# Performance work log

Hardware: AMD Instinct MI355X
Metric: run time of the kernel (lower is better)

Reference implementation:

```python
import jax, jax.numpy as jnp
import numpy as np
from jax.scipy.linalg import solve_triangular

B, N = 8192, 1024  # patch batch, neighborhood size; order=3 -> 10 jet coefficients


def setup_inputs() -> dict:
    key = jax.random.key(0)
    k1, k2 = jax.random.split(key)
    points = jax.random.normal(k1, (B, 3, N), dtype=jnp.float32)
    weights = jax.random.uniform(k2, (B, N), dtype=jnp.float32)
    return {"points": points, "weights": weights}


def fit_wjet_order3(points, weights):
    # points: [B,3,N], weights: [B,N]
    bsz, _, n = points.shape
    x = points[:, 0, :, None]  # [B,N,1]
    y = points[:, 1, :, None]
    z = points[:, 2, :, None]
    w = weights[:, :, None]                      # [B,N,1]
    valid_count = jnp.sum(w > 0.001, axis=1)     # [B,1]
    w_vec = jnp.where(valid_count > 18, weights, jnp.ones_like(weights))[:, :, None]  # [B,N,1]

    # scale normalization h (order > 1 branch)
    h = (jnp.mean(jnp.abs(x), axis=1) + jnp.mean(jnp.abs(y), axis=1)) / 2.0  # [B,1]
    h = jnp.where(jnp.abs(h) < 0.0001, 0.1, h)
    hh = h[:, :, None]                            # [B,1,1]
    x = x / hh
    y = y / hh

    # order-3 polynomial feature matrix A: [B,N,10]
    x_2 = x * x
    y_2 = y * y
    xy = x * y
    A = jnp.concatenate([x, y, x_2, y_2, xy, x_2 * x, y_2 * y, x_2 * y, y_2 * x,
                         jnp.ones_like(x)], axis=2)
    h_2 = h * h
    h_3 = h_2 * h
    d_inv = 1.0 / jnp.concatenate([h, h, h_2, h_2, h_2, h_3, h_3, h_3, h_3,
                                   jnp.ones_like(h)], axis=1)  # [B,10]

    # normal equations (weighted): XtX [B,10,10], XtY [B,10,1]
    XtX = jnp.einsum('bnm,bnk->bmk', A, w_vec * A)
    XtY = jnp.einsum('bnm,bnk->bmk', A, w_vec * z)

    # batched Cholesky solve (happy path of solve_linear_system)
    L = jnp.linalg.cholesky(XtX)
    u = solve_triangular(L, XtY, lower=True)
    beta = solve_triangular(jnp.swapaxes(L, -1, -2), u, lower=False)  # [B,10,1]

    beta = d_inv[:, :, None] * beta  # D_inv @ beta (D_inv is diagonal)

    ones_b1 = jnp.ones((bsz, 1), dtype=beta.dtype)
    n_est = jnp.concatenate([-beta[:, 0:2, 0], ones_b1], axis=1)
    n_est = n_est / jnp.linalg.norm(n_est, axis=1, keepdims=True)

    # analytic neighbor normals (order == 3)
    def bk(k):
        return beta[:, k][:, None, :]  # [B,1,1] broadcasts over N
    nx = -(bk(0) + 2 * bk(2) * x + bk(4) * y + 3 * bk(5) * x_2 + 2 * bk(7) * xy + bk(8) * y_2)
    ny = -(bk(1) + 2 * bk(3) * y + bk(4) * x + 3 * bk(6) * y_2 + bk(7) * x_2 + 2 * bk(8) * xy)
    nn_ = jnp.concatenate([nx, ny, jnp.ones((bsz, n, 1), dtype=beta.dtype)], axis=2)  # [B,N,3]
    neighbor_normals = nn_ / jnp.linalg.norm(nn_, axis=2, keepdims=True)

    return beta[:, :, 0], n_est, neighbor_normals


def reference(points, weights):
    return fit_wjet_order3(points, weights)
```

## Files before the change

kernel.cpp:

```cpp
#include <hip/hip_runtime.h>
#include <math.h>

#define NPTS 1024
#define THREADS 256

template <int CTRL>
__device__ __forceinline__ float dpp_add(float v) {
  int m = __builtin_amdgcn_update_dpp(0, __builtin_bit_cast(int, v), CTRL, 0xF, 0xF, true);
  return v + __builtin_bit_cast(float, m);
}

__device__ __forceinline__ float row_red16(float v) {
  v = dpp_add<0x111>(v);
  v = dpp_add<0x112>(v);
  v = dpp_add<0x114>(v);
  v = dpp_add<0x118>(v);
  return v;
}

__device__ __forceinline__ double rl_f64(double v, int l) {
  typedef int v2i __attribute__((ext_vector_type(2)));
  v2i u = __builtin_bit_cast(v2i, v);
  v2i r;
  r.x = __builtin_amdgcn_readlane(u.x, l);
  r.y = __builtin_amdgcn_readlane(u.y, l);
  return __builtin_bit_cast(double, r);
}

__device__ __forceinline__ float bperm_f(int srclane, float v) {
  return __builtin_bit_cast(float,
      __builtin_amdgcn_ds_bpermute(srclane << 2, __builtin_bit_cast(int, v)));
}

__global__ void __launch_bounds__(THREADS) deepfit_kernel(
    const float* __restrict__ pts, const float* __restrict__ wts,
    float* __restrict__ beta_out, float* __restrict__ nest_out,
    float* __restrict__ nn_out)
{
  const int b = blockIdx.x;
  const int t = threadIdx.x;
  const int lane = t & 63;
  const int wid = t >> 6;

  __shared__ __attribute__((aligned(16))) float s_red[39][16];
  __shared__ int s_cnt[4];
  __shared__ int s_redo;
  __shared__ float s_hw;
  __shared__ float s_beta[10];
  __shared__ double s_L[100];

  const float4* px4 = reinterpret_cast<const float4*>(pts + (size_t)b * (3 * NPTS));
  const float4* pw4 = reinterpret_cast<const float4*>(wts + (size_t)b * NPTS);

  float4 x4 = px4[t];
  float4 y4 = px4[THREADS + t];
  float4 z4 = px4[2 * THREADS + t];
  float4 w4 = pw4[t];

  float xv[4] = {x4.x, x4.y, x4.z, x4.w};
  float yv[4] = {y4.x, y4.y, y4.z, y4.w};
  float zv[4] = {z4.x, z4.y, z4.z, z4.w};
  float wv[4] = {w4.x, w4.y, w4.z, w4.w};

  float habs = 0.f;
  int cnt = 0;
#pragma unroll
  for (int p = 0; p < 4; ++p) {
    habs += fabsf(xv[p]) + fabsf(yv[p]);
    cnt += (int)__popcll(__ballot(wv[p] > 0.001f));
  }
  habs = row_red16(habs);
  if ((lane & 15) == 15) s_red[38][wid * 4 + (lane >> 4)] = habs;
  if (lane == 0) s_cnt[wid] = cnt;

  bool wone = false;
  for (int it = 0; it < 2; ++it) {
    float M[28], Z[10];
#pragma unroll
    for (int i = 0; i < 28; ++i) M[i] = 0.f;
#pragma unroll
    for (int i = 0; i < 10; ++i) Z[i] = 0.f;

#pragma unroll
    for (int p = 0; p < 4; ++p) {
      float x = xv[p];
      float y = yv[p];
      float w = wone ? 1.0f : wv[p];
      float wz = w * zv[p];
      float yp1 = y, yp2 = y * y, yp3 = yp2 * y, yp4 = yp3 * y, yp5 = yp4 * y, yp6 = yp5 * y;
      float tx = w;
      M[0] += tx; M[1] += tx * yp1; M[2] += tx * yp2; M[3] += tx * yp3; M[4] += tx * yp4; M[5] += tx * yp5; M[6] += tx * yp6;
      tx *= x;
      M[7] += tx; M[8] += tx * yp1; M[9] += tx * yp2; M[10] += tx * yp3; M[11] += tx * yp4; M[12] += tx * yp5;
      tx *= x;
      M[13] += tx; M[14] += tx * yp1; M[15] += tx * yp2; M[16] += tx * yp3; M[17] += tx * yp4;
      tx *= x;
      M[18] += tx; M[19] += tx * yp1; M[20] += tx * yp2; M[21] += tx * yp3;
      tx *= x;
      M[22] += tx; M[23] += tx * yp1; M[24] += tx * yp2;
      tx *= x;
      M[25] += tx; M[26] += tx * yp1;
      tx *= x;
      M[27] += tx;
      float tz = wz;
      Z[0] += tz; Z[1] += tz * yp1; Z[2] += tz * yp2; Z[3] += tz * yp3;
      tz *= x;
      Z[4] += tz; Z[5] += tz * yp1; Z[6] += tz * yp2;
      tz *= x;
      Z[7] += tz; Z[8] += tz * yp1;
      tz *= x;
      Z[9] += tz;
    }

#pragma unroll
    for (int i = 0; i < 28; ++i) {
      float v = row_red16(M[i]);
      if ((lane & 15) == 15) s_red[i][wid * 4 + (lane >> 4)] = v;
    }
#pragma unroll
    for (int i = 0; i < 10; ++i) {
      float v = row_red16(Z[i]);
      if ((lane & 15) == 15) s_red[28 + i][wid * 4 + (lane >> 4)] = v;
    }
    __syncthreads();

    if (wid == 0) {
      float rowsum = 0.f;
      if (lane < 39) {
        const float4* r4 = reinterpret_cast<const float4*>(&s_red[lane][0]);
        float4 a0 = r4[0], a1 = r4[1], a2 = r4[2], a3 = r4[3];
        rowsum = ((a0.x + a0.y) + (a0.z + a0.w)) + ((a1.x + a1.y) + (a1.z + a1.w)) +
                 ((a2.x + a2.y) + (a2.z + a2.w)) + ((a3.x + a3.y) + (a3.z + a3.w));
      }
      int ctot = s_cnt[0] + s_cnt[1] + s_cnt[2] + s_cnt[3];
      float hs = __builtin_bit_cast(float,
          __builtin_amdgcn_readlane(__builtin_bit_cast(int, rowsum), 38));
      float mh = hs * (1.0f / 2048.0f);
      if (fabsf(mh) < 1e-4f) mh = 0.1f;
      bool redo = (it == 0) && (ctot <= 18);
      if (lane == 0) { s_redo = redo ? 1 : 0; s_hw = mh; }

      if (!redo) {
        const int lc = (lane < 10) ? lane : 0;
        const int axi = (0x18D21u >> (2 * lc)) & 3;
        const int ayi = (0x27184u >> (2 * lc)) & 3;
        constexpr int AXC[10] = {1, 0, 2, 0, 1, 3, 0, 2, 1, 0};
        constexpr int AYC[10] = {0, 1, 0, 2, 1, 0, 3, 1, 2, 0};
        double a[10], yy;
#pragma unroll
        for (int j = 0; j < 10; ++j) {
          int as = axi + AXC[j];
          int bs = ayi + AYC[j];
          int idx = as * 7 - (as * (as - 1)) / 2 + bs;
          a[j] = (double)bperm_f(idx, rowsum);
        }
        {
          int zi = axi * 4 - (axi * (axi - 1)) / 2 + ayi;
          yy = (double)bperm_f(28 + zi, rowsum);
        }

        if (lane < 10) {
          double Lc[10];
          double rd_own = 1.0;
#pragma unroll
          for (int j = 0; j < 10; ++j) {
            double dj = rl_f64(a[j], j);
            double rdj = 1.0 / dj;
            double lij = a[j] * rdj;
            Lc[j] = lij;
            if (lane == j) rd_own = rdj;
            double wj = rl_f64(yy, j);
            if (lane > j) yy -= lij * wj;
#pragma unroll
            for (int k = j + 1; k < 10; ++k) {
              double ajk = rl_f64(a[k], j);
              a[k] -= lij * ajk;
            }
          }
          yy *= rd_own;
#pragma unroll
          for (int j = 0; j < 10; ++j) s_L[lane * 10 + j] = Lc[j];
          asm volatile("s_waitcnt lgkmcnt(0)" ::: "memory");
#pragma unroll
          for (int j = 9; j >= 0; --j) {
            double xj = rl_f64(yy, j);
            if (lane < j) yy -= s_L[j * 10 + lane] * xj;
          }
          float bf = (float)yy;
          s_beta[lane] = bf;
          beta_out[(size_t)b * 10 + lane] = bf;
          double b0 = rl_f64(yy, 0);
          double b1 = rl_f64(yy, 1);
          if (lane == 0) {
            double invn = 1.0 / sqrt(b0 * b0 + b1 * b1 + 1.0);
            nest_out[(size_t)b * 3 + 0] = (float)(-b0 * invn);
            nest_out[(size_t)b * 3 + 1] = (float)(-b1 * invn);
            nest_out[(size_t)b * 3 + 2] = (float)invn;
          }
        }
      }
    }
    __syncthreads();
    if (s_redo == 0) break;
    wone = true;
  }

  const float h = s_hw;
  const float inv_h = 1.0f / h;
  float bb[10];
#pragma unroll
  for (int i = 0; i < 10; ++i) bb[i] = s_beta[i];
  float nx[4], ny[4], nz[4];
#pragma unroll
  for (int p = 0; p < 4; ++p) {
    float x = xv[p] * inv_h;
    float y = yv[p] * inv_h;
    float x2 = x * x, y2 = y * y, xy = x * y;
    float vx = -(bb[0] + 2.f * bb[2] * x + bb[4] * y + 3.f * bb[5] * x2 + 2.f * bb[7] * xy + bb[8] * y2);
    float vy = -(bb[1] + 2.f * bb[3] * y + bb[4] * x + 3.f * bb[6] * y2 + bb[7] * x2 + 2.f * bb[8] * xy);
    float invn = 1.0f / sqrtf(vx * vx + vy * vy + 1.0f);
    nx[p] = vx * invn; ny[p] = vy * invn; nz[p] = invn;
  }
  {
    float4* o4 = reinterpret_cast<float4*>(nn_out + (size_t)b * (NPTS * 3));
    float4 f0 = make_float4(nx[0], ny[0], nz[0], nx[1]);
    float4 f1 = make_float4(ny[1], nz[1], nx[2], ny[2]);
    float4 f2 = make_float4(nz[2], nx[3], ny[3], nz[3]);
    o4[3 * t + 0] = f0;
    o4[3 * t + 1] = f1;
    o4[3 * t + 2] = f2;
  }
}

extern "C" void kernel_launch(void* const* d_in, const int* in_sizes, int n_in,
                              void* d_out, int out_size, void* d_ws, size_t ws_size,
                              hipStream_t stream) {
  const float* pts = (const float*)d_in[0];
  const float* wts = (const float*)d_in[1];
  float* out = (float*)d_out;
  const int B = in_sizes[1] / NPTS;
  float* beta_out = out;
  float* nest_out = out + (size_t)B * 10;
  float* nn_out = out + (size_t)B * 13;
  deepfit_kernel<<<B, THREADS, 0, stream>>>(pts, wts, beta_out, nest_out, nn_out);
}
```

Measured before the change: 56.08 us.

## Map one patch per wavefront and drop block-level syncs and shared reductions

Each wavefront now handles a whole patch, with four patches per block, instead of a 256-thread block per patch. Reductions use full-wave DPP plus readlane instead of shared-memory partials and __syncthreads. The redo pass re-reads inputs from global memory, and the normal-evaluation stage reloads x and y rather than keeping them in registers. This removes block barriers and the serialized single-wave solve, but makes each lane do four times more accumulation work and adds repeated global loads.

```diff
diff --git a/kernel.cpp b/kernel.cpp
--- a/kernel.cpp
+++ b/kernel.cpp
@@ -2,7 +2,8 @@
 #include <math.h>
 
 #define NPTS 1024
-#define THREADS 256
+#define WPB 4
+#define THREADS (64 * WPB)
 
 template <int CTRL>
 __device__ __forceinline__ float dpp_add(float v) {
@@ -10,12 +11,19 @@
   return v + __builtin_bit_cast(float, m);
 }
 
-__device__ __forceinline__ float row_red16(float v) {
+__device__ __forceinline__ float wave_red_full(float v) {
   v = dpp_add<0x111>(v);
   v = dpp_add<0x112>(v);
   v = dpp_add<0x114>(v);
   v = dpp_add<0x118>(v);
+  v = dpp_add<0x142>(v);
+  v = dpp_add<0x143>(v);
   return v;
+}
+
+__device__ __forceinline__ float red_total(float v) {
+  return __builtin_bit_cast(float,
+      __builtin_amdgcn_readlane(__builtin_bit_cast(int, wave_red_full(v)), 63));
 }
 
 __device__ __forceinline__ double rl_f64(double v, int l) {
@@ -35,200 +43,187 @@
 __global__ void __launch_bounds__(THREADS) deepfit_kernel(
     const float* __restrict__ pts, const float* __restrict__ wts,
     float* __restrict__ beta_out, float* __restrict__ nest_out,
-    float* __restrict__ nn_out)
+    float* __restrict__ nn_out, int B)
 {
-  const int b = blockIdx.x;
-  const int t = threadIdx.x;
-  const int lane = t & 63;
-  const int wid = t >> 6;
-
-  __shared__ __attribute__((aligned(16))) float s_red[39][16];
-  __shared__ int s_cnt[4];
-  __shared__ int s_redo;
-  __shared__ float s_hw;
-  __shared__ float s_beta[10];
-  __shared__ double s_L[100];
+  const int lane = threadIdx.x & 63;
+  const int wid = threadIdx.x >> 6;
+  const int b = blockIdx.x * WPB + wid;
+  if (b >= B) return;
+
+  __shared__ double s_L[WPB][100];
+  double* sL = &s_L[wid][0];
 
   const float4* px4 = reinterpret_cast<const float4*>(pts + (size_t)b * (3 * NPTS));
   const float4* pw4 = reinterpret_cast<const float4*>(wts + (size_t)b * NPTS);
 
-  float4 x4 = px4[t];
-  float4 y4 = px4[THREADS + t];
-  float4 z4 = px4[2 * THREADS + t];
-  float4 w4 = pw4[t];
-
-  float xv[4] = {x4.x, x4.y, x4.z, x4.w};
-  float yv[4] = {y4.x, y4.y, y4.z, y4.w};
-  float zv[4] = {z4.x, z4.y, z4.z, z4.w};
-  float wv[4] = {w4.x, w4.y, w4.z, w4.w};
-
+  float M[28], Z[10];
   float habs = 0.f;
   int cnt = 0;
-#pragma unroll
-  for (int p = 0; p < 4; ++p) {
-    habs += fabsf(xv[p]) + fabsf(yv[p]);
-    cnt += (int)__popcll(__ballot(wv[p] > 0.001f));
-  }
-  habs = row_red16(habs);
-  if ((lane & 15) == 15) s_red[38][wid * 4 + (lane >> 4)] = habs;
-  if (lane == 0) s_cnt[wid] = cnt;
-
-  bool wone = false;
-  for (int it = 0; it < 2; ++it) {
-    float M[28], Z[10];
+
+  for (int pass = 0; pass < 2; ++pass) {
 #pragma unroll
     for (int i = 0; i < 28; ++i) M[i] = 0.f;
 #pragma unroll
     for (int i = 0; i < 10; ++i) Z[i] = 0.f;
 
 #pragma unroll
-    for (int p = 0; p < 4; ++p) {
-      float x = xv[p];
-      float y = yv[p];
-      float w = wone ? 1.0f : wv[p];
-      float wz = w * zv[p];
-      float yp1 = y, yp2 = y * y, yp3 = yp2 * y, yp4 = yp3 * y, yp5 = yp4 * y, yp6 = yp5 * y;
-      float tx = w;
-      M[0] += tx; M[1] += tx * yp1; M[2] += tx * yp2; M[3] += tx * yp3; M[4] += tx * yp4; M[5] += tx * yp5; M[6] += tx * yp6;
-      tx *= x;
-      M[7] += tx; M[8] += tx * yp1; M[9] += tx * yp2; M[10] += tx * yp3; M[11] += tx * yp4; M[12] += tx * yp5;
-      tx *= x;
-      M[13] += tx; M[14] += tx * yp1; M[15] += tx * yp2; M[16] += tx * yp3; M[17] += tx * yp4;
-      tx *= x;
-      M[18] += tx; M[19] += tx * yp1; M[20] += tx * yp2; M[21] += tx * yp3;
-      tx *= x;
-      M[22] += tx; M[23] += tx * yp1; M[24] += tx * yp2;
-      tx *= x;
-      M[25] += tx; M[26] += tx * yp1;
-      tx *= x;
-      M[27] += tx;
-      float tz = wz;
-      Z[0] += tz; Z[1] += tz * yp1; Z[2] += tz * yp2; Z[3] += tz * yp3;
-      tz *= x;
-      Z[4] += tz; Z[5] += tz * yp1; Z[6] += tz * yp2;
-      tz *= x;
-      Z[7] += tz; Z[8] += tz * yp1;
-      tz *= x;
-      Z[9] += tz;
-    }
-
-#pragma unroll
-    for (int i = 0; i < 28; ++i) {
-      float v = row_red16(M[i]);
-      if ((lane & 15) == 15) s_red[i][wid * 4 + (lane >> 4)] = v;
-    }
-#pragma unroll
-    for (int i = 0; i < 10; ++i) {
-      float v = row_red16(Z[i]);
-      if ((lane & 15) == 15) s_red[28 + i][wid * 4 + (lane >> 4)] = v;
-    }
-    __syncthreads();
-
-    if (wid == 0) {
-      float rowsum = 0.f;
-      if (lane < 39) {
-        const float4* r4 = reinterpret_cast<const float4*>(&s_red[lane][0]);
-        float4 a0 = r4[0], a1 = r4[1], a2 = r4[2], a3 = r4[3];
-        rowsum = ((a0.x + a0.y) + (a0.z + a0.w)) + ((a1.x + a1.y) + (a1.z + a1.w)) +
-                 ((a2.x + a2.y) + (a2.z + a2.w)) + ((a3.x + a3.y) + (a3.z + a3.w));
-      }
-      int ctot = s_cnt[0] + s_cnt[1] + s_cnt[2] + s_cnt[3];
-      float hs = __builtin_bit_cast(float,
-          __builtin_amdgcn_readlane(__builtin_bit_cast(int, rowsum), 38));
-      float mh = hs * (1.0f / 2048.0f);
-      if (fabsf(mh) < 1e-4f) mh = 0.1f;
-      bool redo = (it == 0) && (ctot <= 18);
-      if (lane == 0) { s_redo = redo ? 1 : 0; s_hw = mh; }
-
-      if (!redo) {
-        const int lc = (lane < 10) ? lane : 0;
-        const int axi = (0x18D21u >> (2 * lc)) & 3;
-        const int ayi = (0x27184u >> (2 * lc)) & 3;
-        constexpr int AXC[10] = {1, 0, 2, 0, 1, 3, 0, 2, 1, 0};
-        constexpr int AYC[10] = {0, 1, 0, 2, 1, 0, 3, 1, 2, 0};
-        double a[10], yy;
-#pragma unroll
-        for (int j = 0; j < 10; ++j) {
-          int as = axi + AXC[j];
-          int bs = ayi + AYC[j];
-          int idx = as * 7 - (as * (as - 1)) / 2 + bs;
-          a[j] = (double)bperm_f(idx, rowsum);
-        }
-        {
-          int zi = axi * 4 - (axi * (axi - 1)) / 2 + ayi;
-          yy = (double)bperm_f(28 + zi, rowsum);
-        }
-
-        if (lane < 10) {
-          double Lc[10];
-          double rd_own = 1.0;
-#pragma unroll
-          for (int j = 0; j < 10; ++j) {
-            double dj = rl_f64(a[j], j);
-            double rdj = 1.0 / dj;
-            double lij = a[j] * rdj;
-            Lc[j] = lij;
-            if (lane == j) rd_own = rdj;
-            double wj = rl_f64(yy, j);
-            if (lane > j) yy -= lij * wj;
-#pragma unroll
-            for (int k = j + 1; k < 10; ++k) {
-              double ajk = rl_f64(a[k], j);
-              a[k] -= lij * ajk;
-            }
-          }
-          yy *= rd_own;
-#pragma unroll
-          for (int j = 0; j < 10; ++j) s_L[lane * 10 + j] = Lc[j];
-          asm volatile("s_waitcnt lgkmcnt(0)" ::: "memory");
-#pragma unroll
-          for (int j = 9; j >= 0; --j) {
-            double xj = rl_f64(yy, j);
-            if (lane < j) yy -= s_L[j * 10 + lane] * xj;
-          }
-          float bf = (float)yy;
-          s_beta[lane] = bf;
-          beta_out[(size_t)b * 10 + lane] = bf;
-          double b0 = rl_f64(yy, 0);
-          double b1 = rl_f64(yy, 1);
-          if (lane == 0) {
-            double invn = 1.0 / sqrt(b0 * b0 + b1 * b1 + 1.0);
-            nest_out[(size_t)b * 3 + 0] = (float)(-b0 * invn);
-            nest_out[(size_t)b * 3 + 1] = (float)(-b1 * invn);
-            nest_out[(size_t)b * 3 + 2] = (float)invn;
-          }
+    for (int c = 0; c < 4; ++c) {
+      float4 x4 = px4[lane + 64 * c];
+      float4 y4 = px4[256 + lane + 64 * c];
+      float4 z4 = px4[512 + lane + 64 * c];
+      float4 w4 = pw4[lane + 64 * c];
+      float xs[4] = {x4.x, x4.y, x4.z, x4.w};
+      float ys[4] = {y4.x, y4.y, y4.z, y4.w};
+      float zs[4] = {z4.x, z4.y, z4.z, z4.w};
+      float ws[4] = {w4.x, w4.y, w4.z, w4.w};
+      if (pass == 0) {
+#pragma unroll
+        for (int p = 0; p < 4; ++p) {
+          habs += fabsf(xs[p]) + fabsf(ys[p]);
+          cnt += (int)__popcll(__ballot(ws[p] > 0.001f));
         }
       }
-    }
-    __syncthreads();
-    if (s_redo == 0) break;
-    wone = true;
-  }
-
-  const float h = s_hw;
-  const float inv_h = 1.0f / h;
+#pragma unroll
+      for (int p = 0; p < 4; ++p) {
+        float x = xs[p], y = ys[p];
+        float w = (pass == 0) ? ws[p] : 1.0f;
+        float wz = w * zs[p];
+        float yp1 = y, yp2 = y * y, yp3 = yp2 * y, yp4 = yp3 * y, yp5 = yp4 * y, yp6 = yp5 * y;
+        float tx = w;
+        M[0] += tx; M[1] += tx * yp1; M[2] += tx * yp2; M[3] += tx * yp3; M[4] += tx * yp4; M[5] += tx * yp5; M[6] += tx * yp6;
+        tx *= x;
+        M[7] += tx; M[8] += tx * yp1; M[9] += tx * yp2; M[10] += tx * yp3; M[11] += tx * yp4; M[12] += tx * yp5;
+        tx *= x;
+        M[13] += tx; M[14] += tx * yp1; M[15] += tx * yp2; M[16] += tx * yp3; M[17] += tx * yp4;
+        tx *= x;
+        M[18] += tx; M[19] += tx * yp1; M[20] += tx * yp2; M[21] += tx * yp3;
+        tx *= x;
+        M[22] += tx; M[23] += tx * yp1; M[24] += tx * yp2;
+        tx *= x;
+        M[25] += tx; M[26] += tx * yp1;
+        tx *= x;
+        M[27] += tx;
+        float tz = wz;
+        Z[0] += tz; Z[1] += tz * yp1; Z[2] += tz * yp2; Z[3] += tz * yp3;
+        tz *= x;
+        Z[4] += tz; Z[5] += tz * yp1; Z[6] += tz * yp2;
+        tz *= x;
+        Z[7] += tz; Z[8] += tz * yp1;
+        tz *= x;
+        Z[9] += tz;
+      }
+    }
+    if (pass == 1) break;
+    if (cnt > 18) break;
+  }
+
+  float momvec = 0.f;
+#pragma unroll
+  for (int i = 0; i < 28; ++i) {
+    float tot = red_total(M[i]);
+    momvec = (lane == i) ? tot : momvec;
+  }
+#pragma unroll
+  for (int i = 0; i < 10; ++i) {
+    float tot = red_total(Z[i]);
+    momvec = (lane == 28 + i) ? tot : momvec;
+  }
+  float mh;
+  {
+    float htot = red_total(habs);
+    mh = htot * (1.0f / 2048.0f);
+    if (fabsf(mh) < 1e-4f) mh = 0.1f;
+  }
+
+  const int lc = (lane < 10) ? lane : 0;
+  const int axi = (0x18D21u >> (2 * lc)) & 3;
+  const int ayi = (0x27184u >> (2 * lc)) & 3;
+  constexpr int AXC[10] = {1, 0, 2, 0, 1, 3, 0, 2, 1, 0};
+  constexpr int AYC[10] = {0, 1, 0, 2, 1, 0, 3, 1, 2, 0};
+  double a[10], yy;
+#pragma unroll
+  for (int j = 0; j < 10; ++j) {
+    int as = axi + AXC[j];
+    int bs = ayi + AYC[j];
+    int idx = as * 7 - (as * (as - 1)) / 2 + bs;
+    a[j] = (double)bperm_f(idx, momvec);
+  }
+  {
+    int zi = axi * 4 - (axi * (axi - 1)) / 2 + ayi;
+    yy = (double)bperm_f(28 + zi, momvec);
+  }
+
+  float bf = 0.f;
+  if (lane < 10) {
+    double Lc[10];
+    double rd_own = 1.0;
+#pragma unroll
+    for (int j = 0; j < 10; ++j) {
+      double dj = rl_f64(a[j], j);
+      double rdj = 1.0 / dj;
+      double lij = a[j] * rdj;
+      Lc[j] = lij;
+      if (lane == j) rd_own = rdj;
+      double wj = rl_f64(yy, j);
+      if (lane > j) yy -= lij * wj;
+#pragma unroll
+      for (int k = j + 1; k < 10; ++k) {
+        double ajk = rl_f64(a[k], j);
+        a[k] -= lij * ajk;
+      }
+    }
+    yy *= rd_own;
+#pragma unroll
+    for (int j = 0; j < 10; ++j) sL[lane * 10 + j] = Lc[j];
+    asm volatile("s_waitcnt lgkmcnt(0)" ::: "memory");
+    __builtin_amdgcn_sched_barrier(0);
+#pragma unroll
+    for (int j = 9; j >= 0; --j) {
+      double xj = rl_f64(yy, j);
+      if (lane < j) yy -= sL[j * 10 + lane] * xj;
+    }
+    bf = (float)yy;
+    beta_out[(size_t)b * 10 + lane] = bf;
+    double b0 = rl_f64(yy, 0);
+    double b1 = rl_f64(yy, 1);
+    if (lane == 0) {
+      double invn = 1.0 / sqrt(b0 * b0 + b1 * b1 + 1.0);
+      nest_out[(size_t)b * 3 + 0] = (float)(-b0 * invn);
+      nest_out[(size_t)b * 3 + 1] = (float)(-b1 * invn);
+      nest_out[(size_t)b * 3 + 2] = (float)invn;
+    }
+  }
+
   float bb[10];
 #pragma unroll
-  for (int i = 0; i < 10; ++i) bb[i] = s_beta[i];
-  float nx[4], ny[4], nz[4];
-#pragma unroll
-  for (int p = 0; p < 4; ++p) {
-    float x = xv[p] * inv_h;
-    float y = yv[p] * inv_h;
-    float x2 = x * x, y2 = y * y, xy = x * y;
-    float vx = -(bb[0] + 2.f * bb[2] * x + bb[4] * y + 3.f * bb[5] * x2 + 2.f * bb[7] * xy + bb[8] * y2);
-    float vy = -(bb[1] + 2.f * bb[3] * y + bb[4] * x + 3.f * bb[6] * y2 + bb[7] * x2 + 2.f * bb[8] * xy);
-    float invn = 1.0f / sqrtf(vx * vx + vy * vy + 1.0f);
-    nx[p] = vx * invn; ny[p] = vy * invn; nz[p] = invn;
-  }
-  {
-    float4* o4 = reinterpret_cast<float4*>(nn_out + (size_t)b * (NPTS * 3));
+  for (int j = 0; j < 10; ++j)
+    bb[j] = __builtin_bit_cast(float, __builtin_amdgcn_readlane(__builtin_bit_cast(int, bf), j));
+
+  const float inv_h = 1.0f / mh;
+  float4* o4 = reinterpret_cast<float4*>(nn_out + (size_t)b * (NPTS * 3));
+#pragma unroll
+  for (int c = 0; c < 4; ++c) {
+    float4 x4 = px4[lane + 64 * c];
+    float4 y4 = px4[256 + lane + 64 * c];
+    float xs[4] = {x4.x, x4.y, x4.z, x4.w};
+    float ys[4] = {y4.x, y4.y, y4.z, y4.w};
+    float nx[4], ny[4], nz[4];
+#pragma unroll
+    for (int p = 0; p < 4; ++p) {
+      float x = xs[p] * inv_h;
+      float y = ys[p] * inv_h;
+      float x2 = x * x, y2 = y * y, xy = x * y;
+      float vx = -(bb[0] + 2.f * bb[2] * x + bb[4] * y + 3.f * bb[5] * x2 + 2.f * bb[7] * xy + bb[8] * y2);
+      float vy = -(bb[1] + 2.f * bb[3] * y + bb[4] * x + 3.f * bb[6] * y2 + bb[7] * x2 + 2.f * bb[8] * xy);
+      float invn = 1.0f / sqrtf(vx * vx + vy * vy + 1.0f);
+      nx[p] = vx * invn; ny[p] = vy * invn; nz[p] = invn;
+    }
     float4 f0 = make_float4(nx[0], ny[0], nz[0], nx[1]);
     float4 f1 = make_float4(ny[1], nz[1], nx[2], ny[2]);
     float4 f2 = make_float4(nz[2], nx[3], ny[3], nz[3]);
-    o4[3 * t + 0] = f0;
-    o4[3 * t + 1] = f1;
-    o4[3 * t + 2] = f2;
+    o4[192 * c + 3 * lane + 0] = f0;
+    o4[192 * c + 3 * lane + 1] = f1;
+    o4[192 * c + 3 * lane + 2] = f2;
   }
 }
 
@@ -242,5 +237,6 @@
   float* beta_out = out;
   float* nest_out = out + (size_t)B * 10;
   float* nn_out = out + (size_t)B * 13;
-  deepfit_kernel<<<B, THREADS, 0, stream>>>(pts, wts, beta_out, nest_out, nn_out);
-}
+  const int grid = (B + WPB - 1) / WPB;
+  deepfit_kernel<<<grid, THREADS, 0, stream>>>(pts, wts, beta_out, nest_out, nn_out, B);
+}
```

Result: slower. 57.41 us (+2.4%).

## Solve Cholesky redundantly in every wave to remove block barriers

Applied to the files above, without the earlier changes.

Each of the four waves now sums the per-part moment partials from a transposed shared buffer and runs the 10x10 double-precision Cholesky solve itself. Beta is then broadcast by readlane rather than through shared memory, which removes the trailing barrier, the s_beta/s_redo broadcast and the idle waves. The neighbor-normal evaluation folds the 1/h scaling into precomputed coefficients and uses a hardware reciprocal square root. In exchange, every wave repeats the serial f64 solve, and rsq trades a little precision for speed.

```diff
diff --git a/kernel.cpp b/kernel.cpp
--- a/kernel.cpp
+++ b/kernel.cpp
@@ -30,6 +30,14 @@
 __device__ __forceinline__ float bperm_f(int srclane, float v) {
   return __builtin_bit_cast(float,
       __builtin_amdgcn_ds_bpermute(srclane << 2, __builtin_bit_cast(int, v)));
+}
+
+__device__ __forceinline__ float fast_rsq(float x) {
+#if __has_builtin(__builtin_amdgcn_rsqf)
+  return __builtin_amdgcn_rsqf(x);
+#else
+  return 1.0f / sqrtf(x);
+#endif
 }
 
 __global__ void __launch_bounds__(THREADS) deepfit_kernel(
@@ -42,12 +50,10 @@
   const int lane = t & 63;
   const int wid = t >> 6;
 
-  __shared__ __attribute__((aligned(16))) float s_red[39][16];
+  __shared__ float s_red[16][40];
   __shared__ int s_cnt[4];
-  __shared__ int s_redo;
-  __shared__ float s_hw;
-  __shared__ float s_beta[10];
-  __shared__ double s_L[100];
+  __shared__ double s_L[4][100];
+  double* sL = &s_L[wid][0];
 
   const float4* px4 = reinterpret_cast<const float4*>(pts + (size_t)b * (3 * NPTS));
   const float4* pw4 = reinterpret_cast<const float4*>(wts + (size_t)b * NPTS);
@@ -56,12 +62,13 @@
   float4 y4 = px4[THREADS + t];
   float4 z4 = px4[2 * THREADS + t];
   float4 w4 = pw4[t];
-
   float xv[4] = {x4.x, x4.y, x4.z, x4.w};
   float yv[4] = {y4.x, y4.y, y4.z, y4.w};
   float zv[4] = {z4.x, z4.y, z4.z, z4.w};
   float wv[4] = {w4.x, w4.y, w4.z, w4.w};
 
+  const int part = wid * 4 + (lane >> 4);
+
   float habs = 0.f;
   int cnt = 0;
 #pragma unroll
@@ -70,21 +77,22 @@
     cnt += (int)__popcll(__ballot(wv[p] > 0.001f));
   }
   habs = row_red16(habs);
-  if ((lane & 15) == 15) s_red[38][wid * 4 + (lane >> 4)] = habs;
+  if ((lane & 15) == 15) s_red[part][39] = habs;
   if (lane == 0) s_cnt[wid] = cnt;
 
+  float momvec = 0.f;
+  float mh = 0.1f;
   bool wone = false;
   for (int it = 0; it < 2; ++it) {
+    if (it == 1) __syncthreads();
     float M[28], Z[10];
 #pragma unroll
     for (int i = 0; i < 28; ++i) M[i] = 0.f;
 #pragma unroll
     for (int i = 0; i < 10; ++i) Z[i] = 0.f;
-
 #pragma unroll
     for (int p = 0; p < 4; ++p) {
-      float x = xv[p];
-      float y = yv[p];
+      float x = xv[p], y = yv[p];
       float w = wone ? 1.0f : wv[p];
       float wz = w * zv[p];
       float yp1 = y, yp2 = y * y, yp3 = yp2 * y, yp4 = yp3 * y, yp5 = yp4 * y, yp6 = yp5 * y;
@@ -111,114 +119,111 @@
       tz *= x;
       Z[9] += tz;
     }
-
 #pragma unroll
     for (int i = 0; i < 28; ++i) {
       float v = row_red16(M[i]);
-      if ((lane & 15) == 15) s_red[i][wid * 4 + (lane >> 4)] = v;
+      if ((lane & 15) == 15) s_red[part][i] = v;
     }
 #pragma unroll
     for (int i = 0; i < 10; ++i) {
       float v = row_red16(Z[i]);
-      if ((lane & 15) == 15) s_red[28 + i][wid * 4 + (lane >> 4)] = v;
+      if ((lane & 15) == 15) s_red[part][28 + i] = v;
     }
     __syncthreads();
 
-    if (wid == 0) {
-      float rowsum = 0.f;
-      if (lane < 39) {
-        const float4* r4 = reinterpret_cast<const float4*>(&s_red[lane][0]);
-        float4 a0 = r4[0], a1 = r4[1], a2 = r4[2], a3 = r4[3];
-        rowsum = ((a0.x + a0.y) + (a0.z + a0.w)) + ((a1.x + a1.y) + (a1.z + a1.w)) +
-                 ((a2.x + a2.y) + (a2.z + a2.w)) + ((a3.x + a3.y) + (a3.z + a3.w));
+    float acc = 0.f;
+    if (lane < 40) {
+#pragma unroll
+      for (int j = 0; j < 16; ++j) acc += s_red[j][lane];
+    }
+    momvec = acc;
+    {
+      float htot = __builtin_bit_cast(float,
+          __builtin_amdgcn_readlane(__builtin_bit_cast(int, momvec), 39));
+      mh = htot * (1.0f / 2048.0f);
+      if (fabsf(mh) < 1e-4f) mh = 0.1f;
+    }
+    int ctot = s_cnt[0] + s_cnt[1] + s_cnt[2] + s_cnt[3];
+    if (it == 1 || ctot > 18) break;
+    wone = true;
+  }
+
+  const int lc = (lane < 10) ? lane : 0;
+  const int axi = (0x18D21u >> (2 * lc)) & 3;
+  const int ayi = (0x27184u >> (2 * lc)) & 3;
+  constexpr int AXC[10] = {1, 0, 2, 0, 1, 3, 0, 2, 1, 0};
+  constexpr int AYC[10] = {0, 1, 0, 2, 1, 0, 3, 1, 2, 0};
+  double a[10], yy;
+#pragma unroll
+  for (int j = 0; j < 10; ++j) {
+    int as = axi + AXC[j];
+    int bs = ayi + AYC[j];
+    int idx = as * 7 - (as * (as - 1)) / 2 + bs;
+    a[j] = (double)bperm_f(idx, momvec);
+  }
+  {
+    int zi = axi * 4 - (axi * (axi - 1)) / 2 + ayi;
+    yy = (double)bperm_f(28 + zi, momvec);
+  }
+
+  float bf = 0.f;
+  if (lane < 10) {
+    double rd_own = 1.0;
+#pragma unroll
+    for (int j = 0; j < 10; ++j) {
+      double dj = rl_f64(a[j], j);
+      double rdj = 1.0 / dj;
+      double lij = a[j] * rdj;
+      sL[lane * 10 + j] = lij;
+      if (lane == j) rd_own = rdj;
+      double wj = rl_f64(yy, j);
+      if (lane > j) yy -= lij * wj;
+#pragma unroll
+      for (int k = j + 1; k < 10; ++k) {
+        double ajk = rl_f64(a[k], j);
+        a[k] -= lij * ajk;
       }
-      int ctot = s_cnt[0] + s_cnt[1] + s_cnt[2] + s_cnt[3];
-      float hs = __builtin_bit_cast(float,
-          __builtin_amdgcn_readlane(__builtin_bit_cast(int, rowsum), 38));
-      float mh = hs * (1.0f / 2048.0f);
-      if (fabsf(mh) < 1e-4f) mh = 0.1f;
-      bool redo = (it == 0) && (ctot <= 18);
-      if (lane == 0) { s_redo = redo ? 1 : 0; s_hw = mh; }
-
-      if (!redo) {
-        const int lc = (lane < 10) ? lane : 0;
-        const int axi = (0x18D21u >> (2 * lc)) & 3;
-        const int ayi = (0x27184u >> (2 * lc)) & 3;
-        constexpr int AXC[10] = {1, 0, 2, 0, 1, 3, 0, 2, 1, 0};
-        constexpr int AYC[10] = {0, 1, 0, 2, 1, 0, 3, 1, 2, 0};
-        double a[10], yy;
-#pragma unroll
-        for (int j = 0; j < 10; ++j) {
-          int as = axi + AXC[j];
-          int bs = ayi + AYC[j];
-          int idx = as * 7 - (as * (as - 1)) / 2 + bs;
-          a[j] = (double)bperm_f(idx, rowsum);
-        }
-        {
-          int zi = axi * 4 - (axi * (axi - 1)) / 2 + ayi;
-          yy = (double)bperm_f(28 + zi, rowsum);
-        }
-
-        if (lane < 10) {
-          double Lc[10];
-          double rd_own = 1.0;
-#pragma unroll
-          for (int j = 0; j < 10; ++j) {
-            double dj = rl_f64(a[j], j);
-            double rdj = 1.0 / dj;
-            double lij = a[j] * rdj;
-            Lc[j] = lij;
-            if (lane == j) rd_own = rdj;
-            double wj = rl_f64(yy, j);
-            if (lane > j) yy -= lij * wj;
-#pragma unroll
-            for (int k = j + 1; k < 10; ++k) {
-              double ajk = rl_f64(a[k], j);
-              a[k] -= lij * ajk;
-            }
-          }
-          yy *= rd_own;
-#pragma unroll
-          for (int j = 0; j < 10; ++j) s_L[lane * 10 + j] = Lc[j];
-          asm volatile("s_waitcnt lgkmcnt(0)" ::: "memory");
-#pragma unroll
-          for (int j = 9; j >= 0; --j) {
-            double xj = rl_f64(yy, j);
-            if (lane < j) yy -= s_L[j * 10 + lane] * xj;
-          }
-          float bf = (float)yy;
-          s_beta[lane] = bf;
-          beta_out[(size_t)b * 10 + lane] = bf;
-          double b0 = rl_f64(yy, 0);
-          double b1 = rl_f64(yy, 1);
-          if (lane == 0) {
-            double invn = 1.0 / sqrt(b0 * b0 + b1 * b1 + 1.0);
-            nest_out[(size_t)b * 3 + 0] = (float)(-b0 * invn);
-            nest_out[(size_t)b * 3 + 1] = (float)(-b1 * invn);
-            nest_out[(size_t)b * 3 + 2] = (float)invn;
-          }
-        }
-      }
-    }
-    __syncthreads();
-    if (s_redo == 0) break;
-    wone = true;
-  }
-
-  const float h = s_hw;
-  const float inv_h = 1.0f / h;
+    }
+    yy *= rd_own;
+    asm volatile("s_waitcnt lgkmcnt(0)" ::: "memory");
+    __builtin_amdgcn_sched_barrier(0);
+#pragma unroll
+    for (int j = 9; j >= 0; --j) {
+      double xj = rl_f64(yy, j);
+      if (lane < j) yy -= sL[j * 10 + lane] * xj;
+    }
+    bf = (float)yy;
+    if (wid == 0) beta_out[(size_t)b * 10 + lane] = bf;
+    if (wid == 0 && lane == 0) {
+      double b0 = yy;
+      double b1 = rl_f64(yy, 1);
+      b1 = rl_f64(yy, 1);
+      double invn = 1.0 / sqrt(b0 * b0 + b1 * b1 + 1.0);
+      nest_out[(size_t)b * 3 + 0] = (float)(-b0 * invn);
+      nest_out[(size_t)b * 3 + 1] = (float)(-b1 * invn);
+      nest_out[(size_t)b * 3 + 2] = (float)invn;
+    }
+  }
+
   float bb[10];
 #pragma unroll
-  for (int i = 0; i < 10; ++i) bb[i] = s_beta[i];
+  for (int j = 0; j < 10; ++j)
+    bb[j] = __builtin_bit_cast(float, __builtin_amdgcn_readlane(__builtin_bit_cast(int, bf), j));
+  const float ih = 1.0f / mh;
+  const float ih2 = ih * ih;
+  const float u0 = bb[0], u2 = 2.f * bb[2] * ih, u4 = bb[4] * ih;
+  const float u5 = 3.f * bb[5] * ih2, u7 = 2.f * bb[7] * ih2, u8 = bb[8] * ih2;
+  const float v1 = bb[1], v3 = 2.f * bb[3] * ih, v4 = bb[4] * ih;
+  const float v6 = 3.f * bb[6] * ih2, v7 = bb[7] * ih2, v8 = 2.f * bb[8] * ih2;
+
   float nx[4], ny[4], nz[4];
 #pragma unroll
   for (int p = 0; p < 4; ++p) {
-    float x = xv[p] * inv_h;
-    float y = yv[p] * inv_h;
+    float x = xv[p], y = yv[p];
     float x2 = x * x, y2 = y * y, xy = x * y;
-    float vx = -(bb[0] + 2.f * bb[2] * x + bb[4] * y + 3.f * bb[5] * x2 + 2.f * bb[7] * xy + bb[8] * y2);
-    float vy = -(bb[1] + 2.f * bb[3] * y + bb[4] * x + 3.f * bb[6] * y2 + bb[7] * x2 + 2.f * bb[8] * xy);
-    float invn = 1.0f / sqrtf(vx * vx + vy * vy + 1.0f);
+    float vx = -(u0 + u2 * x + u4 * y + u5 * x2 + u7 * xy + u8 * y2);
+    float vy = -(v1 + v3 * y + v4 * x + v6 * y2 + v7 * x2 + v8 * xy);
+    float invn = fast_rsq(vx * vx + vy * vy + 1.0f);
     nx[p] = vx * invn; ny[p] = vy * invn; nz[p] = invn;
   }
   {
```

New measurement: 61.88 us. 1.1x slower.
